# Kernel tuning notes

Hardware: AMD Instinct MI355X
Metric: run time of the kernel (lower is better)

The kernel has to match this reference:

```python
import jax, jax.numpy as jnp
import numpy as np

B, L, IN, H, DEPTH, FH, NE, OUT = 8, 4096, 3, 512, 8, 64, 8, 2

def _layernorm(x, g, b, eps=1e-5):
    m = jnp.mean(x, axis=-1, keepdims=True)
    v = jnp.mean(jnp.square(x - m), axis=-1, keepdims=True)
    return (x - m) * jax.lax.rsqrt(v + eps) * g + b

def setup_inputs() -> dict:
    key = jax.random.key(0)
    ks = iter(jax.random.split(key, 32))
    def n(shape, s=0.02):
        return jax.random.normal(next(ks), shape, jnp.float32) * s
    inp = {
        'x': jax.random.normal(next(ks), (B, L, IN), jnp.float32),
        'edge_ids': jax.random.randint(next(ks), (B,), 0, NE),
        'in_w': n((IN, H)), 'in_b': jnp.zeros((H,), jnp.float32),
        'edge_emb': n((NE, H)),
        # per-block params, stacked over depth
        'ln_g': jnp.ones((DEPTH, H), jnp.float32), 'ln_b': jnp.zeros((DEPTH, H), jnp.float32),
        'fw1': n((DEPTH, 1, FH), 0.5), 'fb1': jnp.zeros((DEPTH, FH), jnp.float32),
        'fw2': n((DEPTH, FH, FH), 0.1), 'fb2': jnp.zeros((DEPTH, FH), jnp.float32),
        'fw3': n((DEPTH, FH, H), 0.1), 'fb3': jnp.zeros((DEPTH, H), jnp.float32),
        'cw': n((DEPTH, H, 3), 0.3), 'cb': jnp.zeros((DEPTH, H), jnp.float32),
        'win_w': n((DEPTH, H, 3 * H)), 'win_b': jnp.zeros((DEPTH, 3 * H), jnp.float32),
        'wout_w': n((DEPTH, H, H)), 'wout_b': jnp.zeros((DEPTH, H), jnp.float32),
        'fln_g': jnp.ones((H,), jnp.float32), 'fln_b': jnp.zeros((H,), jnp.float32),
        'hw1': n((H, H // 2)), 'hb1': jnp.zeros((H // 2,), jnp.float32),
        'hw2': n((H // 2, OUT)), 'hb2': jnp.zeros((OUT,), jnp.float32),
    }
    return inp

def reference(x, edge_ids, in_w, in_b, edge_emb, ln_g, ln_b, fw1, fb1, fw2, fb2,
              fw3, fb3, cw, cb, win_w, win_b, wout_w, wout_b, fln_g, fln_b,
              hw1, hb1, hw2, hb2):
    b, seq, _ = x.shape
    Hd = in_w.shape[1]
    h = x @ in_w + in_b  # (B,L,H)
    # sinusoidal positional encoding (interleaved sin/cos)
    pos = jnp.arange(seq, dtype=jnp.float32)[:, None]
    div = jnp.exp(jnp.arange(0, Hd, 2, dtype=jnp.float32) * (-np.log(10000.0) / Hd))
    pe = jnp.stack([jnp.sin(pos * div), jnp.cos(pos * div)], axis=-1).reshape(seq, Hd)
    h = h + pe[None] + edge_emb[edge_ids][:, None, :]
    t = jnp.linspace(0.0, 1.0, seq, dtype=jnp.float32)[:, None]  # (L,1)
    depth = ln_g.shape[0]
    for i in range(depth):
        hn = _layernorm(h, ln_g[i], ln_b[i])
        proj = hn @ win_w[i] + win_b[i]  # (B,L,3H)
        v, u, z = jnp.split(proj, 3, axis=-1)
        # implicit filter MLP (exact GELU as in nn.GELU)
        f = jax.nn.gelu(t @ fw1[i] + fb1[i], approximate=False)
        f = jax.nn.gelu(f @ fw2[i] + fb2[i], approximate=False)
        filt = f @ fw3[i] + fb3[i]  # (L,H)
        # depthwise short conv, kernel=3, padding=1
        up = jnp.pad(u, ((0, 0), (1, 1), (0, 0)))
        us = (up[:, :-2] * cw[i][:, 0] + up[:, 1:-1] * cw[i][:, 1]
              + up[:, 2:] * cw[i][:, 2] + cb[i])
        # FFT long convolution over sequence dim
        U = jnp.fft.rfft(us, axis=1)
        Ft = jnp.fft.rfft(filt, n=seq, axis=0)
        filtered = jnp.fft.irfft(U * Ft[None], n=seq, axis=1)
        out = v * filtered * jax.nn.sigmoid(z)  # gate (order>=2)
        h = h + (out @ wout_w[i] + wout_b[i])  # dropout = identity (eval)
    h = _layernorm(h, fln_g, fln_b)
    h = jax.nn.gelu(h @ hw1 + hb1, approximate=False)
    return h @ hw2 + hb2  # (B,L,OUT)
```

## Files before the change

kernel.cpp:

```cpp
#include <hip/hip_runtime.h>
#include <hip/hip_bf16.h>


typedef short bf16x8 __attribute__((ext_vector_type(8)));
typedef float f32x4 __attribute__((ext_vector_type(4)));

__device__ __forceinline__ float bf2f(short s) {
    return __uint_as_float(((unsigned)(unsigned short)s) << 16);
}
__device__ __forceinline__ short f2bf(float f) {
    __hip_bfloat16 h = __float2bfloat16(f);
    return *reinterpret_cast<short*>(&h);
}
__device__ __forceinline__ float gelu_exact(float x) {
    return 0.5f * x * (1.0f + erff(x * 0.70710678118654752f));
}
__device__ __forceinline__ float sigmoidf_(float x) {
    return 1.0f / (1.0f + expf(-x));
}
__device__ __forceinline__ float2 cmul(float2 a, float2 b) {
    return make_float2(a.x*b.x - a.y*b.y, a.x*b.y + a.y*b.x);
}
__device__ __forceinline__ float2 cmulc(float2 a, float2 b) {
    return make_float2(a.x*b.x + a.y*b.y, a.y*b.x - a.x*b.y);
}

__device__ __forceinline__ void gload_lds16(const void* gsrc, void* ldsdst) {
    __builtin_amdgcn_global_load_lds(
        (const __attribute__((address_space(1))) void*)gsrc,
        (__attribute__((address_space(3))) void*)ldsdst, 16, 0, 0);
}

__global__ __launch_bounds__(256)
void embed_kernel(const float* __restrict__ x, const int* __restrict__ eids,
                  const float* __restrict__ in_w, const float* __restrict__ in_b,
                  const float* __restrict__ eemb, float* __restrict__ h)
{
    const int bl = blockIdx.x;
    const int b  = bl >> 12;
    const int l  = bl & 4095;
    const float x0 = x[bl*3 + 0], x1 = x[bl*3 + 1], x2 = x[bl*3 + 2];
    const int e = eids[b];
    #pragma unroll
    for (int i = 0; i < 2; ++i) {
        int col = threadIdx.x + 256*i;
        int k = col >> 1;
        float dv = expf(-0.03597789207803197f * (float)k);
        float ang = (float)l * dv;
        float pe = (col & 1) ? cosf(ang) : sinf(ang);
        float val = x0*in_w[col] + x1*in_w[512 + col] + x2*in_w[1024 + col]
                  + in_b[col] + pe + eemb[e*512 + col];
        h[(size_t)bl*512 + col] = val;
    }
}

__global__ __launch_bounds__(256)
void ln_kernel(const float* __restrict__ hsrc, const float* __restrict__ g,
               const float* __restrict__ bta, short* __restrict__ out)
{
    const int m = blockIdx.x * 4 + (threadIdx.x >> 6);
    const int lane = threadIdx.x & 63;
    const float4* hp = (const float4*)(hsrc + (size_t)m * 512);
    float4 v0 = hp[lane*2], v1 = hp[lane*2 + 1];
    float xs[8] = {v0.x, v0.y, v0.z, v0.w, v1.x, v1.y, v1.z, v1.w};
    float s = 0.f, sq = 0.f;
    #pragma unroll
    for (int i = 0; i < 8; ++i) { s += xs[i]; sq += xs[i]*xs[i]; }
    #pragma unroll
    for (int o = 32; o > 0; o >>= 1) { s += __shfl_xor(s, o); sq += __shfl_xor(sq, o); }
    float mean = s * (1.f/512.f);
    float var  = sq * (1.f/512.f) - mean*mean;
    float rs = rsqrtf(var + 1e-5f);
    short res[8];
    #pragma unroll
    for (int i = 0; i < 8; ++i) {
        int col = lane*8 + i;
        res[i] = f2bf((xs[i] - mean) * rs * g[col] + bta[col]);
    }
    *(bf16x8*)(out + (size_t)m*512 + lane*8) = *(bf16x8*)res;
}

template<int EPI>
__global__ __launch_bounds__(256)
void gemm_bf16(const short* __restrict__ A, const short* __restrict__ Bt,
               const float* __restrict__ bias, short* __restrict__ Cb,
               float* __restrict__ Cres, int N, int K)
{
    __shared__ __align__(16) short As[128 * 64];
    __shared__ __align__(16) short Bs[128 * 64];
    const int tid = threadIdx.x;
    const int w = tid >> 6, lane = tid & 63;
    const int m0 = blockIdx.x * 128, n0 = blockIdx.y * 128;
    const int wm = w >> 1, wn = w & 1;
    const int lane15 = lane & 15, lhi = lane >> 4;

    f32x4 acc[4][4];
    #pragma unroll
    for (int i = 0; i < 4; ++i)
        #pragma unroll
        for (int j = 0; j < 4; ++j) acc[i][j] = (f32x4){0.f, 0.f, 0.f, 0.f};

    for (int k0 = 0; k0 < K; k0 += 64) {
        #pragma unroll
        for (int i = 0; i < 4; ++i) {
            int row = 32*w + 8*i + (lane >> 3);
            int kch = (lane & 7) ^ (row & 7);
            gload_lds16(A + (size_t)(m0 + row) * K + k0 + kch*8, &As[(32*w + 8*i) * 64]);
        }
        #pragma unroll
        for (int i = 0; i < 4; ++i) {
            int row = 32*w + 8*i + (lane >> 3);
            int kch = (lane & 7) ^ (row & 7);
            gload_lds16(Bt + (size_t)(n0 + row) * K + k0 + kch*8, &Bs[(32*w + 8*i) * 64]);
        }
        __syncthreads();
        #pragma unroll
        for (int kk = 0; kk < 64; kk += 32) {
            bf16x8 af[4], bfr[4];
            const int kb = kk + lhi * 8;
            #pragma unroll
            for (int mi = 0; mi < 4; ++mi) {
                int row = wm*64 + mi*16 + lane15;
                af[mi] = *(const bf16x8*)&As[(row*64 + kb) ^ ((row & 7) << 3)];
            }
            #pragma unroll
            for (int ni = 0; ni < 4; ++ni) {
                int row = wn*64 + ni*16 + lane15;
                bfr[ni] = *(const bf16x8*)&Bs[(row*64 + kb) ^ ((row & 7) << 3)];
            }
            #pragma unroll
            for (int mi = 0; mi < 4; ++mi)
                #pragma unroll
                for (int ni = 0; ni < 4; ++ni)
                    acc[mi][ni] = __builtin_amdgcn_mfma_f32_16x16x32_bf16(
                        af[mi], bfr[ni], acc[mi][ni], 0, 0, 0);
        }
        __syncthreads();
    }
    #pragma unroll
    for (int mi = 0; mi < 4; ++mi) {
        #pragma unroll
        for (int ni = 0; ni < 4; ++ni) {
            int gcol = n0 + wn*64 + ni*16 + lane15;
            float bv = bias[gcol];
            #pragma unroll
            for (int r = 0; r < 4; ++r) {
                int grow = m0 + wm*64 + mi*16 + lhi*4 + r;
                float val = acc[mi][ni][r] + bv;
                if (EPI == 0) {
                    Cb[(size_t)grow * N + gcol] = f2bf(val);
                } else if (EPI == 1) {
                    float* p = Cres + (size_t)grow * N + gcol;
                    *p += val;
                } else {
                    Cb[(size_t)grow * N + gcol] = f2bf(gelu_exact(val));
                }
            }
        }
    }
}

__global__ __launch_bounds__(256)
void mlp_kernel(const float* __restrict__ fw1, const float* __restrict__ fb1,
                const float* __restrict__ fw2, const float* __restrict__ fb2,
                const float* __restrict__ fw3, const float* __restrict__ fb3,
                float* __restrict__ filt_t)
{
    __shared__ float F1[64][65];
    __shared__ float F2[64][65];
    __shared__ float FO[64][129];
    const int lt = blockIdx.x, ns = blockIdx.y;
    const int l0 = lt * 64, nb = ns * 128;
    const int tid = threadIdx.x;
    for (int i = tid; i < 4096; i += 256) {
        int l = i >> 6, j = i & 63;
        float tv = (float)(l0 + l) * (1.0f / 4095.0f);
        F1[l][j] = gelu_exact(tv * fw1[j] + fb1[j]);
    }
    __syncthreads();
    {
        int j = tid & 63, lb = tid >> 6;
        for (int li = 0; li < 16; ++li) {
            int l = lb*16 + li;
            float sum = fb2[j];
            #pragma unroll
            for (int k = 0; k < 64; ++k) sum += F1[l][k] * fw2[k*64 + j];
            F2[l][j] = gelu_exact(sum);
        }
    }
    __syncthreads();
    {
        const int nn = tid & 127;
        const int lofs = tid >> 7;
        for (int jj = 0; jj < 32; ++jj) {
            int l = lofs + 2*jj;
            float sum = fb3[nb + nn];
            #pragma unroll
            for (int k = 0; k < 64; ++k) sum += F2[l][k] * fw3[k*512 + nb + nn];
            FO[l][nn] = sum;
        }
    }
    __syncthreads();
    for (int i = tid; i < 8192; i += 256) {
        int nn = i >> 6, l = i & 63;
        filt_t[(size_t)(nb + nn) * 4096 + l0 + l] = FO[l][nn];
    }
}

__global__ __launch_bounds__(256)
void convT_kernel(const short* __restrict__ proj, const float* __restrict__ cw,
                  const float* __restrict__ cb, short* __restrict__ ust)
{
    __shared__ float U[66][65];
    __shared__ float O[64][65];
    const int lt = blockIdx.x, ht = blockIdx.y, b = blockIdx.z;
    const int l0 = lt * 64, h0 = ht * 64;
    const int tid = threadIdx.x;
    const int c63 = tid & 63, r4 = tid >> 6;
    for (int r = r4; r < 66; r += 4) {
        int l = l0 - 1 + r;
        float v = 0.f;
        if (l >= 0 && l < 4096)
            v = bf2f(proj[((size_t)(b*4096 + l)) * 1536 + 512 + h0 + c63]);
        U[r][c63] = v;
    }
    __syncthreads();
    const int hcol = h0 + c63;
    const float c0 = cw[hcol*3], c1 = cw[hcol*3+1], c2 = cw[hcol*3+2];
    const float cbv = cb[hcol];
    #pragma unroll
    for (int j = 0; j < 16; ++j) {
        int r = r4 + 4*j;
        O[r][c63] = U[r][c63]*c0 + U[r+1][c63]*c1 + U[r+2][c63]*c2 + cbv;
    }
    __syncthreads();
    for (int j = 0; j < 16; ++j) {
        int hh = r4 + 4*j;
        ust[((size_t)(b*512 + h0 + hh)) * 4096 + l0 + c63] = f2bf(O[c63][hh]);
    }
}

#define FIDX(i) ((i) + ((i) >> 4))

template<int MODE>
__global__ __launch_bounds__(256)
void fft_kernel(const float* __restrict__ rin_f, const short* __restrict__ rin_h,
                const float2* __restrict__ Fh, short* __restrict__ rout_h,
                float2* __restrict__ Fout, const float2* __restrict__ tw)
{
    __shared__ float2 S[4096 + 256];
    const int tid = threadIdx.x;
    const int hh = blockIdx.x;
    if (MODE == 0) {
        const float* src = rin_f + (size_t)hh * 4096;
        for (int i = tid; i < 4096; i += 256) S[FIDX(i)] = make_float2(src[i], 0.f);
    } else {
        const int b0 = blockIdx.y * 2, b1 = b0 + 1;
        const short* s0 = rin_h + ((size_t)b0 * 512 + hh) * 4096;
        const short* s1 = rin_h + ((size_t)b1 * 512 + hh) * 4096;
        for (int i = tid; i < 4096; i += 256)
            S[FIDX(i)] = make_float2(bf2f(s0[i]), bf2f(s1[i]));
    }
    __syncthreads();
    #pragma unroll
    for (int s = 0; s < 6; ++s) {
        const int lq = 10 - 2*s;
        const int q = 1 << lq;
        const int tf = 1 << (2*s);
        for (int bfy = tid; bfy < 1024; bfy += 256) {
            const int j = bfy & (q - 1);
            const int base = ((bfy >> lq) << (lq + 2)) + j;
            float2 a = S[FIDX(base)];
            float2 b = S[FIDX(base + q)];
            float2 c = S[FIDX(base + 2*q)];
            float2 d = S[FIDX(base + 3*q)];
            float2 t0 = make_float2(a.x + c.x, a.y + c.y);
            float2 t1 = make_float2(a.x - c.x, a.y - c.y);
            float2 t2 = make_float2(b.x + d.x, b.y + d.y);
            float2 t3 = make_float2(b.x - d.x, b.y - d.y);
            float2 o0 = make_float2(t0.x + t2.x, t0.y + t2.y);
            float2 p1 = make_float2(t1.x + t3.y, t1.y - t3.x);
            float2 p2 = make_float2(t0.x - t2.x, t0.y - t2.y);
            float2 p3 = make_float2(t1.x - t3.y, t1.y + t3.x);
            S[FIDX(base)]       = o0;
            S[FIDX(base + q)]   = cmul(p1, tw[j * tf]);
            S[FIDX(base + 2*q)] = cmul(p2, tw[2 * j * tf]);
            S[FIDX(base + 3*q)] = cmul(p3, tw[3 * j * tf]);
        }
        __syncthreads();
    }
    if (MODE == 0) {
        float2* dst = Fout + (size_t)hh * 4096;
        for (int i = tid; i < 4096; i += 256) dst[i] = S[FIDX(i)];
        return;
    }
    const float2* F = Fh + (size_t)hh * 4096;
    #pragma unroll
    for (int s = 0; s < 6; ++s) {
        const int q = 1 << (2*s);
        const int tf = 1 << (10 - 2*s);
        for (int bfy = tid; bfy < 1024; bfy += 256) {
            const int j = bfy & (q - 1);
            const int base = ((bfy >> (2*s)) << (2*s + 2)) + j;
            float2 u0 = S[FIDX(base)];
            float2 u1 = S[FIDX(base + q)];
            float2 u2 = S[FIDX(base + 2*q)];
            float2 u3 = S[FIDX(base + 3*q)];
            if (s == 0) {
                u0 = cmul(u0, F[base]);     u1 = cmul(u1, F[base + 1]);
                u2 = cmul(u2, F[base + 2]); u3 = cmul(u3, F[base + 3]);
            } else {
                u1 = cmulc(u1, tw[j * tf]);
                u2 = cmulc(u2, tw[2 * j * tf]);
                u3 = cmulc(u3, tw[3 * j * tf]);
            }
            float2 pp = make_float2(u0.x + u2.x, u0.y + u2.y);
            float2 mm = make_float2(u0.x - u2.x, u0.y - u2.y);
            float2 rr = make_float2(u1.x + u3.x, u1.y + u3.y);
            float2 tt = make_float2(u1.x - u3.x, u1.y - u3.y);
            S[FIDX(base)]       = make_float2(pp.x + rr.x, pp.y + rr.y);
            S[FIDX(base + q)]   = make_float2(mm.x - tt.y, mm.y + tt.x);
            S[FIDX(base + 2*q)] = make_float2(pp.x - rr.x, pp.y - rr.y);
            S[FIDX(base + 3*q)] = make_float2(mm.x + tt.y, mm.y - tt.x);
        }
        __syncthreads();
    }
    const int b0 = blockIdx.y * 2, b1 = b0 + 1;
    short* d0 = rout_h + ((size_t)b0 * 512 + hh) * 4096;
    short* d1 = rout_h + ((size_t)b1 * 512 + hh) * 4096;
    const float inv = 1.0f / 4096.0f;
    for (int i = tid; i < 4096; i += 256) {
        float2 v = S[FIDX(i)];
        d0[i] = f2bf(v.x * inv);
        d1[i] = f2bf(v.y * inv);
    }
}

__global__ __launch_bounds__(256)
void gateT_kernel(const short* __restrict__ ft, const short* __restrict__ proj,
                  short* __restrict__ gated)
{
    __shared__ float Fd[64][65];
    const int lt = blockIdx.x, ht = blockIdx.y, b = blockIdx.z;
    const int l0 = lt * 64, h0 = ht * 64;
    const int tid = threadIdx.x, c63 = tid & 63, r4 = tid >> 6;
    for (int j = 0; j < 16; ++j) {
        int hh = r4 + 4*j;
        Fd[hh][c63] = bf2f(ft[((size_t)(b*512 + h0 + hh)) * 4096 + l0 + c63]);
    }
    __syncthreads();
    for (int j = 0; j < 16; ++j) {
        int l = l0 + r4 + 4*j;
        size_t mrow = (size_t)(b*4096 + l) * 1536;
        float v = bf2f(proj[mrow + h0 + c63]);
        float z = bf2f(proj[mrow + 1024 + h0 + c63]);
        float f = Fd[c63][r4 + 4*j];
        gated[(size_t)(b*4096 + l) * 512 + h0 + c63] = f2bf(v * f * sigmoidf_(z));
    }
}

__global__ __launch_bounds__(256)
void transpose_cvt(const float* __restrict__ in, short* __restrict__ out, int R, int C)
{
    __shared__ float T[32][33];
    const float* ip = in;
    short* op = out;
    int tx = threadIdx.x & 31, ty = threadIdx.x >> 5;
    int r0 = blockIdx.y * 32, c0 = blockIdx.x * 32;
    for (int j = 0; j < 4; ++j)
        T[ty + 8*j][tx] = ip[(size_t)(r0 + ty + 8*j) * C + c0 + tx];
    __syncthreads();
    for (int j = 0; j < 4; ++j)
        op[(size_t)(c0 + ty + 8*j) * R + r0 + tx] = f2bf(T[tx][ty + 8*j]);
}

__global__ void twiddle_kernel(float2* tw)
{
    int k = blockIdx.x * 256 + threadIdx.x;
    if (k < 4096) {
        float ang = -(float)(6.283185307179586 / 4096.0) * (float)k;
        tw[k] = make_float2(cosf(ang), sinf(ang));
    }
}

__global__ __launch_bounds__(256)
void head_kernel(const short* __restrict__ g2, const float* __restrict__ hw2,
                 const float* __restrict__ hb2, float* __restrict__ out)
{
    const int m = blockIdx.x * 4 + (threadIdx.x >> 6);
    const int lane = threadIdx.x & 63;
    const short* row = g2 + (size_t)m * 256;
    float a0 = 0.f, a1 = 0.f;
    #pragma unroll
    for (int i = 0; i < 4; ++i) {
        int k = lane*4 + i;
        float gv = bf2f(row[k]);
        a0 += gv * hw2[2*k];
        a1 += gv * hw2[2*k + 1];
    }
    #pragma unroll
    for (int o = 32; o > 0; o >>= 1) { a0 += __shfl_xor(a0, o); a1 += __shfl_xor(a1, o); }
    if (lane == 0) {
        out[(size_t)m*2]     = a0 + hb2[0];
        out[(size_t)m*2 + 1] = a1 + hb2[1];
    }
}

extern "C" void kernel_launch(void* const* d_in, const int* in_sizes, int n_in,
                              void* d_out, int out_size, void* d_ws, size_t ws_size,
                              hipStream_t stream)
{
    const float* x      = (const float*)d_in[0];
    const int*   eids   = (const int*)d_in[1];
    const float* in_w   = (const float*)d_in[2];
    const float* in_b   = (const float*)d_in[3];
    const float* eemb   = (const float*)d_in[4];
    const float* ln_g   = (const float*)d_in[5];
    const float* ln_b   = (const float*)d_in[6];
    const float* fw1    = (const float*)d_in[7];
    const float* fb1    = (const float*)d_in[8];
    const float* fw2    = (const float*)d_in[9];
    const float* fb2    = (const float*)d_in[10];
    const float* fw3    = (const float*)d_in[11];
    const float* fb3    = (const float*)d_in[12];
    const float* cw     = (const float*)d_in[13];
    const float* cb     = (const float*)d_in[14];
    const float* win_w  = (const float*)d_in[15];
    const float* win_b  = (const float*)d_in[16];
    const float* wout_w = (const float*)d_in[17];
    const float* wout_b = (const float*)d_in[18];
    const float* fln_g  = (const float*)d_in[19];
    const float* fln_b  = (const float*)d_in[20];
    const float* hw1    = (const float*)d_in[21];
    const float* hb1    = (const float*)d_in[22];
    const float* hw2    = (const float*)d_in[23];
    const float* hb2    = (const float*)d_in[24];
    float* out = (float*)d_out;

    char* p = (char*)d_ws;
    auto alloc = [&](size_t bytes) { char* r = p; p += (bytes + 255) & ~(size_t)255; return r; };
    float2* tw    = (float2*)alloc((size_t)4096 * sizeof(float2));
    short*  winT  = (short*)alloc((size_t)1536 * 512 * 2);
    short*  woutT = (short*)alloc((size_t)512 * 512 * 2);
    short*  hw1T  = (short*)alloc((size_t)256 * 512 * 2);
    float*  h     = (float*)alloc((size_t)32768 * 512 * 4);
    short*  hn    = (short*)alloc((size_t)32768 * 512 * 2);
    short*  proj  = (short*)alloc((size_t)32768 * 1536 * 2);
    short*  ust   = (short*)alloc((size_t)8 * 512 * 4096 * 2);
    float*  filt  = (float*)ust;
    float2* Fh    = (float2*)alloc((size_t)512 * 4096 * sizeof(float2));

    twiddle_kernel<<<16, 256, 0, stream>>>(tw);
    transpose_cvt<<<dim3(256/32, 512/32), 256, 0, stream>>>(hw1, hw1T, 512, 256);
    embed_kernel<<<32768, 256, 0, stream>>>(x, eids, in_w, in_b, eemb, h);

    for (int d = 0; d < 8; ++d) {
        transpose_cvt<<<dim3(1536/32, 512/32), 256, 0, stream>>>(
            win_w + (size_t)d*512*1536, winT, 512, 1536);
        transpose_cvt<<<dim3(512/32, 512/32), 256, 0, stream>>>(
            wout_w + (size_t)d*512*512, woutT, 512, 512);
        mlp_kernel<<<dim3(64, 4), 256, 0, stream>>>(
            fw1 + d*64, fb1 + d*64, fw2 + (size_t)d*64*64, fb2 + d*64,
            fw3 + (size_t)d*64*512, fb3 + d*512, filt);
        fft_kernel<0><<<512, 256, 0, stream>>>(filt, nullptr, nullptr, nullptr, Fh, tw);
        ln_kernel<<<8192, 256, 0, stream>>>(h, ln_g + d*512, ln_b + d*512, hn);
        gemm_bf16<0><<<dim3(256, 12), 256, 0, stream>>>(
            hn, winT, win_b + d*1536, proj, nullptr, 1536, 512);
        convT_kernel<<<dim3(64, 8, 8), 256, 0, stream>>>(
            proj, cw + (size_t)d*512*3, cb + d*512, ust);
        fft_kernel<1><<<dim3(512, 4), 256, 0, stream>>>(nullptr, ust, Fh, ust, nullptr, tw);
        gateT_kernel<<<dim3(64, 8, 8), 256, 0, stream>>>(ust, proj, hn);
        gemm_bf16<1><<<dim3(256, 4), 256, 0, stream>>>(
            hn, woutT, wout_b + d*512, nullptr, h, 512, 512);
    }

    ln_kernel<<<8192, 256, 0, stream>>>(h, fln_g, fln_b, hn);
    gemm_bf16<2><<<dim3(256, 2), 256, 0, stream>>>(hn, hw1T, hb1, proj, nullptr, 256, 512);
    head_kernel<<<8192, 256, 0, stream>>>(proj, hw2, hb2, out);
}
```

Measured before the change: 2.800 ms.

## Split input projection into transposed-u GEMM and fused v*sigmoid(z) GEMM

The 1536-wide input projection is split in two. One GEMM computes only the u slice and writes it already transposed to (B,H,L) through shared memory. A second GEMM computes v and z together and writes v*sigmoid(z) directly. The depthwise short convolution moves into the FFT kernel's load stage, so the standalone conv/transpose kernel and the full proj buffer are no longer needed, and the gate kernel now reads one narrow tensor. Weight transposes for all depths are also hoisted out of the layer loop into single batched launches. The vz GEMM holds two accumulator sets, which raises register pressure.

```diff
diff --git a/kernel.cpp b/kernel.cpp
--- a/kernel.cpp
+++ b/kernel.cpp
@@ -147,14 +147,183 @@
             for (int r = 0; r < 4; ++r) {
                 int grow = m0 + wm*64 + mi*16 + lhi*4 + r;
                 float val = acc[mi][ni][r] + bv;
-                if (EPI == 0) {
-                    Cb[(size_t)grow * N + gcol] = f2bf(val);
-                } else if (EPI == 1) {
+                if (EPI == 1) {
                     float* p = Cres + (size_t)grow * N + gcol;
                     *p += val;
                 } else {
                     Cb[(size_t)grow * N + gcol] = f2bf(gelu_exact(val));
                 }
+            }
+        }
+    }
+}
+
+__global__ __launch_bounds__(256)
+void gemm_u(const short* __restrict__ A, const short* __restrict__ Bt,
+            const float* __restrict__ bias, short* __restrict__ ut)
+{
+    __shared__ __align__(16) short smem[128 * 128];
+    short* As = smem;
+    short* Bs = smem + 128*64;
+    const int tid = threadIdx.x;
+    const int w = tid >> 6, lane = tid & 63;
+    const int m0 = blockIdx.x * 128, n0 = blockIdx.y * 128;
+    const int wm = w >> 1, wn = w & 1;
+    const int lane15 = lane & 15, lhi = lane >> 4;
+    const int K = 512;
+
+    f32x4 acc[4][4];
+    #pragma unroll
+    for (int i = 0; i < 4; ++i)
+        #pragma unroll
+        for (int j = 0; j < 4; ++j) acc[i][j] = (f32x4){0.f, 0.f, 0.f, 0.f};
+
+    for (int k0 = 0; k0 < K; k0 += 64) {
+        #pragma unroll
+        for (int i = 0; i < 4; ++i) {
+            int row = 32*w + 8*i + (lane >> 3);
+            int kch = (lane & 7) ^ (row & 7);
+            gload_lds16(A + (size_t)(m0 + row) * K + k0 + kch*8, &As[(32*w + 8*i) * 64]);
+        }
+        #pragma unroll
+        for (int i = 0; i < 4; ++i) {
+            int row = 32*w + 8*i + (lane >> 3);
+            int kch = (lane & 7) ^ (row & 7);
+            gload_lds16(Bt + (size_t)(n0 + row) * K + k0 + kch*8, &Bs[(32*w + 8*i) * 64]);
+        }
+        __syncthreads();
+        #pragma unroll
+        for (int kk = 0; kk < 64; kk += 32) {
+            bf16x8 af[4], bfr[4];
+            const int kb = kk + lhi * 8;
+            #pragma unroll
+            for (int mi = 0; mi < 4; ++mi) {
+                int row = wm*64 + mi*16 + lane15;
+                af[mi] = *(const bf16x8*)&As[(row*64 + kb) ^ ((row & 7) << 3)];
+            }
+            #pragma unroll
+            for (int ni = 0; ni < 4; ++ni) {
+                int row = wn*64 + ni*16 + lane15;
+                bfr[ni] = *(const bf16x8*)&Bs[(row*64 + kb) ^ ((row & 7) << 3)];
+            }
+            #pragma unroll
+            for (int mi = 0; mi < 4; ++mi)
+                #pragma unroll
+                for (int ni = 0; ni < 4; ++ni)
+                    acc[mi][ni] = __builtin_amdgcn_mfma_f32_16x16x32_bf16(
+                        af[mi], bfr[ni], acc[mi][ni], 0, 0, 0);
+        }
+        __syncthreads();
+    }
+    #pragma unroll
+    for (int mi = 0; mi < 4; ++mi) {
+        #pragma unroll
+        for (int ni = 0; ni < 4; ++ni) {
+            int hcol = wn*64 + ni*16 + lane15;
+            float bv = bias[n0 + hcol];
+            #pragma unroll
+            for (int r = 0; r < 4; ++r) {
+                int bl = wm*64 + mi*16 + lhi*4 + r;
+                smem[hcol*128 + (bl ^ ((hcol & 7) << 3))] = f2bf(acc[mi][ni][r] + bv);
+            }
+        }
+    }
+    __syncthreads();
+    const int b = m0 >> 12, l0 = m0 & 4095;
+    #pragma unroll
+    for (int p = 0; p < 8; ++p) {
+        int hh = p*16 + (tid >> 4);
+        int lbase = (tid & 15) * 8;
+        bf16x8 v = *(const bf16x8*)&smem[hh*128 + (lbase ^ ((hh & 7) << 3))];
+        *(bf16x8*)(ut + ((size_t)(b*512 + n0 + hh))*4096 + l0 + lbase) = v;
+    }
+}
+
+__global__ __launch_bounds__(256)
+void gemm_vz(const short* __restrict__ A, const short* __restrict__ BtW,
+             const float* __restrict__ biasW, short* __restrict__ G)
+{
+    __shared__ __align__(16) short As[128 * 64];
+    __shared__ __align__(16) short Bv[128 * 64];
+    __shared__ __align__(16) short Bz[128 * 64];
+    const int tid = threadIdx.x;
+    const int w = tid >> 6, lane = tid & 63;
+    const int m0 = blockIdx.x * 128, n0 = blockIdx.y * 128;
+    const int wm = w >> 1, wn = w & 1;
+    const int lane15 = lane & 15, lhi = lane >> 4;
+    const int K = 512;
+    const short* BtZ = BtW + (size_t)1024 * 512;
+
+    f32x4 av[4][4], az[4][4];
+    #pragma unroll
+    for (int i = 0; i < 4; ++i)
+        #pragma unroll
+        for (int j = 0; j < 4; ++j) {
+            av[i][j] = (f32x4){0.f, 0.f, 0.f, 0.f};
+            az[i][j] = (f32x4){0.f, 0.f, 0.f, 0.f};
+        }
+
+    for (int k0 = 0; k0 < K; k0 += 64) {
+        #pragma unroll
+        for (int i = 0; i < 4; ++i) {
+            int row = 32*w + 8*i + (lane >> 3);
+            int kch = (lane & 7) ^ (row & 7);
+            gload_lds16(A + (size_t)(m0 + row) * K + k0 + kch*8, &As[(32*w + 8*i) * 64]);
+        }
+        #pragma unroll
+        for (int i = 0; i < 4; ++i) {
+            int row = 32*w + 8*i + (lane >> 3);
+            int kch = (lane & 7) ^ (row & 7);
+            gload_lds16(BtW + (size_t)(n0 + row) * K + k0 + kch*8, &Bv[(32*w + 8*i) * 64]);
+        }
+        #pragma unroll
+        for (int i = 0; i < 4; ++i) {
+            int row = 32*w + 8*i + (lane >> 3);
+            int kch = (lane & 7) ^ (row & 7);
+            gload_lds16(BtZ + (size_t)(n0 + row) * K + k0 + kch*8, &Bz[(32*w + 8*i) * 64]);
+        }
+        __syncthreads();
+        #pragma unroll
+        for (int kk = 0; kk < 64; kk += 32) {
+            bf16x8 af[4], bfv[4], bfz[4];
+            const int kb = kk + lhi * 8;
+            #pragma unroll
+            for (int mi = 0; mi < 4; ++mi) {
+                int row = wm*64 + mi*16 + lane15;
+                af[mi] = *(const bf16x8*)&As[(row*64 + kb) ^ ((row & 7) << 3)];
+            }
+            #pragma unroll
+            for (int ni = 0; ni < 4; ++ni) {
+                int row = wn*64 + ni*16 + lane15;
+                int idx = (row*64 + kb) ^ ((row & 7) << 3);
+                bfv[ni] = *(const bf16x8*)&Bv[idx];
+                bfz[ni] = *(const bf16x8*)&Bz[idx];
+            }
+            #pragma unroll
+            for (int mi = 0; mi < 4; ++mi)
+                #pragma unroll
+                for (int ni = 0; ni < 4; ++ni) {
+                    av[mi][ni] = __builtin_amdgcn_mfma_f32_16x16x32_bf16(
+                        af[mi], bfv[ni], av[mi][ni], 0, 0, 0);
+                    az[mi][ni] = __builtin_amdgcn_mfma_f32_16x16x32_bf16(
+                        af[mi], bfz[ni], az[mi][ni], 0, 0, 0);
+                }
+        }
+        __syncthreads();
+    }
+    #pragma unroll
+    for (int mi = 0; mi < 4; ++mi) {
+        #pragma unroll
+        for (int ni = 0; ni < 4; ++ni) {
+            int gcol = n0 + wn*64 + ni*16 + lane15;
+            float bvv = biasW[gcol];
+            float bzz = biasW[1024 + gcol];
+            #pragma unroll
+            for (int r = 0; r < 4; ++r) {
+                int grow = m0 + wm*64 + mi*16 + lhi*4 + r;
+                float vv = av[mi][ni][r] + bvv;
+                float zz = az[mi][ni][r] + bzz;
+                G[(size_t)grow * 512 + gcol] = f2bf(vv * sigmoidf_(zz));
             }
         }
     }
@@ -207,46 +376,14 @@
     }
 }
 
-__global__ __launch_bounds__(256)
-void convT_kernel(const short* __restrict__ proj, const float* __restrict__ cw,
-                  const float* __restrict__ cb, short* __restrict__ ust)
-{
-    __shared__ float U[66][65];
-    __shared__ float O[64][65];
-    const int lt = blockIdx.x, ht = blockIdx.y, b = blockIdx.z;
-    const int l0 = lt * 64, h0 = ht * 64;
-    const int tid = threadIdx.x;
-    const int c63 = tid & 63, r4 = tid >> 6;
-    for (int r = r4; r < 66; r += 4) {
-        int l = l0 - 1 + r;
-        float v = 0.f;
-        if (l >= 0 && l < 4096)
-            v = bf2f(proj[((size_t)(b*4096 + l)) * 1536 + 512 + h0 + c63]);
-        U[r][c63] = v;
-    }
-    __syncthreads();
-    const int hcol = h0 + c63;
-    const float c0 = cw[hcol*3], c1 = cw[hcol*3+1], c2 = cw[hcol*3+2];
-    const float cbv = cb[hcol];
-    #pragma unroll
-    for (int j = 0; j < 16; ++j) {
-        int r = r4 + 4*j;
-        O[r][c63] = U[r][c63]*c0 + U[r+1][c63]*c1 + U[r+2][c63]*c2 + cbv;
-    }
-    __syncthreads();
-    for (int j = 0; j < 16; ++j) {
-        int hh = r4 + 4*j;
-        ust[((size_t)(b*512 + h0 + hh)) * 4096 + l0 + c63] = f2bf(O[c63][hh]);
-    }
-}
-
 #define FIDX(i) ((i) + ((i) >> 4))
 
 template<int MODE>
 __global__ __launch_bounds__(256)
 void fft_kernel(const float* __restrict__ rin_f, const short* __restrict__ rin_h,
                 const float2* __restrict__ Fh, short* __restrict__ rout_h,
-                float2* __restrict__ Fout, const float2* __restrict__ tw)
+                float2* __restrict__ Fout, const float2* __restrict__ tw,
+                const float* __restrict__ cw3, const float* __restrict__ cbv)
 {
     __shared__ float2 S[4096 + 256];
     const int tid = threadIdx.x;
@@ -254,14 +391,31 @@
     if (MODE == 0) {
         const float* src = rin_f + (size_t)hh * 4096;
         for (int i = tid; i < 4096; i += 256) S[FIDX(i)] = make_float2(src[i], 0.f);
+        __syncthreads();
     } else {
         const int b0 = blockIdx.y * 2, b1 = b0 + 1;
         const short* s0 = rin_h + ((size_t)b0 * 512 + hh) * 4096;
         const short* s1 = rin_h + ((size_t)b1 * 512 + hh) * 4096;
         for (int i = tid; i < 4096; i += 256)
             S[FIDX(i)] = make_float2(bf2f(s0[i]), bf2f(s1[i]));
-    }
-    __syncthreads();
+        __syncthreads();
+        const float c0 = cw3[hh*3 + 0], c1 = cw3[hh*3 + 1], c2 = cw3[hh*3 + 2];
+        const float cb = cbv[hh];
+        float2 r[16];
+        #pragma unroll
+        for (int k = 0; k < 16; ++k) {
+            int i = tid + 256*k;
+            float2 um = (i == 0)    ? make_float2(0.f, 0.f) : S[FIDX(i-1)];
+            float2 uc = S[FIDX(i)];
+            float2 up = (i == 4095) ? make_float2(0.f, 0.f) : S[FIDX(i+1)];
+            r[k] = make_float2(um.x*c0 + uc.x*c1 + up.x*c2 + cb,
+                               um.y*c0 + uc.y*c1 + up.y*c2 + cb);
+        }
+        __syncthreads();
+        #pragma unroll
+        for (int k = 0; k < 16; ++k) S[FIDX(tid + 256*k)] = r[k];
+        __syncthreads();
+    }
     #pragma unroll
     for (int s = 0; s < 6; ++s) {
         const int lq = 10 - 2*s;
@@ -337,7 +491,7 @@
 }
 
 __global__ __launch_bounds__(256)
-void gateT_kernel(const short* __restrict__ ft, const short* __restrict__ proj,
+void gateT_kernel(const short* __restrict__ ft, const short* __restrict__ g,
                   short* __restrict__ gated)
 {
     __shared__ float Fd[64][65];
@@ -351,11 +505,10 @@
     __syncthreads();
     for (int j = 0; j < 16; ++j) {
         int l = l0 + r4 + 4*j;
-        size_t mrow = (size_t)(b*4096 + l) * 1536;
-        float v = bf2f(proj[mrow + h0 + c63]);
-        float z = bf2f(proj[mrow + 1024 + h0 + c63]);
+        size_t row = (size_t)(b*4096 + l) * 512;
+        float gv = bf2f(g[row + h0 + c63]);
         float f = Fd[c63][r4 + 4*j];
-        gated[(size_t)(b*4096 + l) * 512 + h0 + c63] = f2bf(v * f * sigmoidf_(z));
+        gated[row + h0 + c63] = f2bf(gv * f);
     }
 }
 
@@ -363,8 +516,9 @@
 void transpose_cvt(const float* __restrict__ in, short* __restrict__ out, int R, int C)
 {
     __shared__ float T[32][33];
-    const float* ip = in;
-    short* op = out;
+    const size_t off = (size_t)blockIdx.z * R * C;
+    const float* ip = in + off;
+    short* op = out + off;
     int tx = threadIdx.x & 31, ty = threadIdx.x >> 5;
     int r0 = blockIdx.y * 32, c0 = blockIdx.x * 32;
     for (int j = 0; j < 4; ++j)
@@ -439,42 +593,44 @@
 
     char* p = (char*)d_ws;
     auto alloc = [&](size_t bytes) { char* r = p; p += (bytes + 255) & ~(size_t)255; return r; };
-    float2* tw    = (float2*)alloc((size_t)4096 * sizeof(float2));
-    short*  winT  = (short*)alloc((size_t)1536 * 512 * 2);
-    short*  woutT = (short*)alloc((size_t)512 * 512 * 2);
-    short*  hw1T  = (short*)alloc((size_t)256 * 512 * 2);
-    float*  h     = (float*)alloc((size_t)32768 * 512 * 4);
-    short*  hn    = (short*)alloc((size_t)32768 * 512 * 2);
-    short*  proj  = (short*)alloc((size_t)32768 * 1536 * 2);
-    short*  ust   = (short*)alloc((size_t)8 * 512 * 4096 * 2);
-    float*  filt  = (float*)ust;
-    float2* Fh    = (float2*)alloc((size_t)512 * 4096 * sizeof(float2));
+    float2* tw     = (float2*)alloc((size_t)4096 * sizeof(float2));
+    short*  winT8  = (short*)alloc((size_t)8 * 1536 * 512 * 2);
+    short*  woutT8 = (short*)alloc((size_t)8 * 512 * 512 * 2);
+    short*  hw1T   = (short*)alloc((size_t)256 * 512 * 2);
+    float*  h      = (float*)alloc((size_t)32768 * 512 * 4);
+    short*  hn     = (short*)alloc((size_t)32768 * 512 * 2);
+    short*  g      = (short*)alloc((size_t)32768 * 512 * 2);
+    short*  ut     = (short*)alloc((size_t)8 * 512 * 4096 * 2);
+    float*  filt   = (float*)ut;
+    float2* Fh     = (float2*)alloc((size_t)512 * 4096 * sizeof(float2));
 
     twiddle_kernel<<<16, 256, 0, stream>>>(tw);
-    transpose_cvt<<<dim3(256/32, 512/32), 256, 0, stream>>>(hw1, hw1T, 512, 256);
+    transpose_cvt<<<dim3(48, 16, 8), 256, 0, stream>>>(win_w, winT8, 512, 1536);
+    transpose_cvt<<<dim3(16, 16, 8), 256, 0, stream>>>(wout_w, woutT8, 512, 512);
+    transpose_cvt<<<dim3(8, 16, 1), 256, 0, stream>>>(hw1, hw1T, 512, 256);
     embed_kernel<<<32768, 256, 0, stream>>>(x, eids, in_w, in_b, eemb, h);
 
     for (int d = 0; d < 8; ++d) {
-        transpose_cvt<<<dim3(1536/32, 512/32), 256, 0, stream>>>(
-            win_w + (size_t)d*512*1536, winT, 512, 1536);
-        transpose_cvt<<<dim3(512/32, 512/32), 256, 0, stream>>>(
-            wout_w + (size_t)d*512*512, woutT, 512, 512);
+        const short* winTd = winT8 + (size_t)d * 1536 * 512;
         mlp_kernel<<<dim3(64, 4), 256, 0, stream>>>(
             fw1 + d*64, fb1 + d*64, fw2 + (size_t)d*64*64, fb2 + d*64,
             fw3 + (size_t)d*64*512, fb3 + d*512, filt);
-        fft_kernel<0><<<512, 256, 0, stream>>>(filt, nullptr, nullptr, nullptr, Fh, tw);
+        fft_kernel<0><<<512, 256, 0, stream>>>(
+            filt, nullptr, nullptr, nullptr, Fh, tw, nullptr, nullptr);
         ln_kernel<<<8192, 256, 0, stream>>>(h, ln_g + d*512, ln_b + d*512, hn);
-        gemm_bf16<0><<<dim3(256, 12), 256, 0, stream>>>(
-            hn, winT, win_b + d*1536, proj, nullptr, 1536, 512);
-        convT_kernel<<<dim3(64, 8, 8), 256, 0, stream>>>(
-            proj, cw + (size_t)d*512*3, cb + d*512, ust);
-        fft_kernel<1><<<dim3(512, 4), 256, 0, stream>>>(nullptr, ust, Fh, ust, nullptr, tw);
-        gateT_kernel<<<dim3(64, 8, 8), 256, 0, stream>>>(ust, proj, hn);
+        gemm_u<<<dim3(256, 4), 256, 0, stream>>>(
+            hn, winTd + (size_t)512*512, win_b + d*1536 + 512, ut);
+        gemm_vz<<<dim3(256, 4), 256, 0, stream>>>(
+            hn, winTd, win_b + d*1536, g);
+        fft_kernel<1><<<dim3(512, 4), 256, 0, stream>>>(
+            nullptr, ut, Fh, ut, nullptr, tw, cw + (size_t)d*512*3, cb + d*512);
+        gateT_kernel<<<dim3(64, 8, 8), 256, 0, stream>>>(ut, g, hn);
         gemm_bf16<1><<<dim3(256, 4), 256, 0, stream>>>(
-            hn, woutT, wout_b + d*512, nullptr, h, 512, 512);
+            hn, woutT8 + (size_t)d*512*512, wout_b + d*512, nullptr, h, 512, 512);
     }
 
     ln_kernel<<<8192, 256, 0, stream>>>(h, fln_g, fln_b, hn);
-    gemm_bf16<2><<<dim3(256, 2), 256, 0, stream>>>(hn, hw1T, hb1, proj, nullptr, 256, 512);
-    head_kernel<<<8192, 256, 0, stream>>>(proj, hw2, hb2, out);
-}
+    gemm_bf16<2><<<dim3(256, 2), 256, 0, stream>>>(
+        hn, hw1T, hb1, (short*)g, nullptr, 256, 512);
+    head_kernel<<<8192, 256, 0, stream>>>((short*)g, hw2, hb2, out);
+}
```

Measured after the change: 2.771 ms. No clear change (-1.1%).
